# Kernel optimization log

Hardware: AMD Instinct MI355X
Metric: run time of the kernel (lower is better)

Reference implementation:

```python
import jax, jax.numpy as jnp
import numpy as np

B, T, D_IN, D_OUT = 4, 2048, 1024, 1024

def setup_inputs() -> dict:
    key = jax.random.key(0)
    k1, k2, k3, k4 = jax.random.split(key, 4)
    return {
        "vector": jax.random.normal(k1, (B, T, D_IN), dtype=jnp.float32),
        "W_queries": jax.random.normal(k2, (D_IN, D_OUT), dtype=jnp.float32),
        "W_keys": jax.random.normal(k3, (D_IN, D_OUT), dtype=jnp.float32),
        "W_values": jax.random.normal(k4, (D_IN, D_OUT), dtype=jnp.float32),
    }

def reference(vector, W_queries, W_keys, W_values):
    # vector: [B,T,d_in]; projections -> [B,T,d_out]
    q = vector @ W_queries
    k = vector @ W_keys
    v = vector @ W_values
    d_out = k.shape[-1]
    scores = jnp.einsum('btd,bsd->bts', q, k)  # [B,T,T]
    t = scores.shape[1]
    causal = jnp.tril(jnp.ones((t, t), dtype=bool))  # True = keep (mask is triu diag=1)
    scores = jnp.where(causal, scores, -jnp.inf)
    weights = jax.nn.softmax(scores / jnp.sqrt(jnp.float32(d_out)), axis=-1)
    # dropout p=0.0 -> identity
    return jnp.einsum('bts,bsd->btd', weights, v)
```

## Files before the change

### kernel.cpp

```cpp
#include <hip/hip_runtime.h>

#define TT   2048
#define DD   1024
#define BK   32

typedef float  f32x4  __attribute__((ext_vector_type(4)));
typedef __bf16 bf16x8 __attribute__((ext_vector_type(8)));

static __device__ __forceinline__ unsigned short f2bf(float f){
  unsigned int u = __float_as_uint(f);
  return (unsigned short)((u + 0x7fffu + ((u >> 16) & 1u)) >> 16);
}
static __device__ __forceinline__ float bf2f(unsigned short h){
  return __uint_as_float(((unsigned int)h) << 16);
}
static __device__ __forceinline__ bf16x8 ld8(const unsigned short* p){
  return *(const bf16x8*)p;
}
static __device__ __forceinline__ f32x4 mfma16(bf16x8 a, bf16x8 b, f32x4 c){
  return __builtin_amdgcn_mfma_f32_16x16x32_bf16(a, b, c, 0, 0, 0);
}

static __device__ __forceinline__ void async16(
    const unsigned short* g, unsigned short* l)
{
  __builtin_amdgcn_global_load_lds(
      (const __attribute__((address_space(1))) unsigned int*)g,
      (__attribute__((address_space(3))) unsigned int*)l, 16, 0, 0);
}

static __device__ __forceinline__ void stage_async(
    const unsigned short* __restrict__ src, int row_stride,
    unsigned short* __restrict__ dst, int t)
{
#pragma unroll
  for (int j = 0; j < 2; j++){
    int e = (t + j * 256) * 8;
    int row = e >> 5, col = e & 31;
    async16(src + (size_t)row * row_stride + col, dst + e);
  }
}

__global__ __launch_bounds__(256) void split_all_kernel(
    const float* __restrict__ X,  const float* __restrict__ Wq,
    const float* __restrict__ Wk, const float* __restrict__ Wv,
    unsigned short* __restrict__ Xhi,  unsigned short* __restrict__ Xlo,
    unsigned short* __restrict__ Wqhi, unsigned short* __restrict__ Wqlo,
    unsigned short* __restrict__ Wkhi, unsigned short* __restrict__ Wklo,
    unsigned short* __restrict__ WvThi)
{
  __shared__ float tile[32][33];
  int bx = blockIdx.x;
  if (bx < 10240){
    const float* src; unsigned short *hi, *lo; size_t base;
    if (bx < 8192)      { src = X;  hi = Xhi;  lo = Xlo;  base = (size_t)bx * 1024; }
    else if (bx < 9216) { src = Wq; hi = Wqhi; lo = Wqlo; base = (size_t)(bx - 8192) * 1024; }
    else                { src = Wk; hi = Wkhi; lo = Wklo; base = (size_t)(bx - 9216) * 1024; }
    size_t i = base + (size_t)threadIdx.x * 4;
    const float4 x = *(const float4*)(src + i);
    ushort4 h, l;
    h.x = f2bf(x.x); l.x = f2bf(x.x - bf2f(h.x));
    h.y = f2bf(x.y); l.y = f2bf(x.y - bf2f(h.y));
    h.z = f2bf(x.z); l.z = f2bf(x.z - bf2f(h.z));
    h.w = f2bf(x.w); l.w = f2bf(x.w - bf2f(h.w));
    *(ushort4*)(hi + i) = h;
    *(ushort4*)(lo + i) = l;
  } else {
    int tid = bx - 10240;
    int k0 = (tid & 31) * 32, n0 = (tid >> 5) * 32;
    int tx = threadIdx.x & 31, ty = threadIdx.x >> 5;
#pragma unroll
    for (int r = 0; r < 4; r++){
      int row = ty + r * 8;
      tile[row][tx] = Wv[(size_t)(k0 + row) * DD + n0 + tx];
    }
    __syncthreads();
#pragma unroll
    for (int r = 0; r < 4; r++){
      int nrow = ty + r * 8;
      float v = tile[tx][nrow];
      WvThi[(size_t)(n0 + nrow) * DD + k0 + tx] = f2bf(v);
    }
  }
}

__global__ __launch_bounds__(256) void mt_kernel(
    const unsigned short* __restrict__ Wkhi, const unsigned short* __restrict__ Wklo,
    const unsigned short* __restrict__ Wqhi, const unsigned short* __restrict__ Wqlo,
    unsigned short* __restrict__ MThi, unsigned short* __restrict__ MTlo)
{
  __shared__ unsigned short Ahi[128 * BK], Alo[128 * BK];
  __shared__ unsigned short Bhi[128 * BK], Blo[128 * BK];
  int e0 = blockIdx.y * 128, d0 = blockIdx.x * 128;
  const unsigned short* Ah_g = Wkhi + (size_t)e0 * DD;
  const unsigned short* Al_g = Wklo + (size_t)e0 * DD;
  const unsigned short* Bh_g = Wqhi + (size_t)d0 * DD;
  const unsigned short* Bl_g = Wqlo + (size_t)d0 * DD;
  int t = threadIdx.x;
  int lane = t & 63, w = t >> 6;
  int mw = (w >> 1) << 6, nw = (w & 1) << 6;
  int frow = lane & 15, fk = (lane >> 4) << 3;

  f32x4 acc[4][4];
#pragma unroll
  for (int a = 0; a < 4; a++)
#pragma unroll
    for (int c = 0; c < 4; c++){ f32x4 zz = {0.f,0.f,0.f,0.f}; acc[a][c] = zz; }

  for (int kk = 0; kk < DD / BK; kk++){
    int k0 = kk * BK;
    stage_async(Ah_g + k0, DD, Ahi, t);
    stage_async(Al_g + k0, DD, Alo, t);
    stage_async(Bh_g + k0, DD, Bhi, t);
    stage_async(Bl_g + k0, DD, Blo, t);
    __syncthreads();

    bf16x8 ah[4], al[4], bh[4], bl[4];
#pragma unroll
    for (int tm = 0; tm < 4; tm++){
      int off = (mw + tm * 16 + frow) * BK + fk;
      ah[tm] = ld8(&Ahi[off]); al[tm] = ld8(&Alo[off]);
    }
#pragma unroll
    for (int tn = 0; tn < 4; tn++){
      int off = (nw + tn * 16 + frow) * BK + fk;
      bh[tn] = ld8(&Bhi[off]); bl[tn] = ld8(&Blo[off]);
    }
#pragma unroll
    for (int tm = 0; tm < 4; tm++)
#pragma unroll
      for (int tn = 0; tn < 4; tn++){
        acc[tm][tn] = mfma16(ah[tm], bh[tn], acc[tm][tn]);
        acc[tm][tn] = mfma16(ah[tm], bl[tn], acc[tm][tn]);
        acc[tm][tn] = mfma16(al[tm], bh[tn], acc[tm][tn]);
      }
    __syncthreads();
  }

#pragma unroll
  for (int tm = 0; tm < 4; tm++)
#pragma unroll
    for (int tn = 0; tn < 4; tn++)
#pragma unroll
      for (int r = 0; r < 4; r++){
        float v = acc[tm][tn][r];
        int ge = e0 + mw + tm * 16 + ((lane >> 4) << 2) + r;
        int gd = d0 + nw + tn * 16 + frow;
        size_t idx = (size_t)ge * DD + gd;
        unsigned short h = f2bf(v);
        MThi[idx] = h; MTlo[idx] = f2bf(v - bf2f(h));
      }
}

__global__ __launch_bounds__(256, 2) void y_kernel(
    const unsigned short* __restrict__ Xhi, const unsigned short* __restrict__ Xlo,
    const unsigned short* __restrict__ MThi, const unsigned short* __restrict__ MTlo,
    const unsigned short* __restrict__ WvThi,
    unsigned short* __restrict__ Yhi, unsigned short* __restrict__ Ylo,
    unsigned short* __restrict__ VT)
{
  __shared__ unsigned short Ahs[128 * BK], Als[128 * BK];
  __shared__ unsigned short Bmh[128 * BK], Bml[128 * BK], Bvh[128 * BK];
  int m0 = blockIdx.x * 128, n0 = blockIdx.y * 128;
  const unsigned short* Ah_g  = Xhi   + (size_t)m0 * DD;
  const unsigned short* Al_g  = Xlo   + (size_t)m0 * DD;
  const unsigned short* Bmh_g = MThi  + (size_t)n0 * DD;
  const unsigned short* Bml_g = MTlo  + (size_t)n0 * DD;
  const unsigned short* Bvh_g = WvThi + (size_t)n0 * DD;
  int t = threadIdx.x;
  int lane = t & 63, w = t >> 6;
  int mw = (w >> 1) << 6, nw = (w & 1) << 6;
  int frow = lane & 15, fk = (lane >> 4) << 3;

  f32x4 accY[4][4], accV[4][4];
#pragma unroll
  for (int a = 0; a < 4; a++)
#pragma unroll
    for (int c = 0; c < 4; c++){
      f32x4 zz = {0.f,0.f,0.f,0.f}; accY[a][c] = zz; accV[a][c] = zz;
    }

  for (int kk = 0; kk < DD / BK; kk++){
    int k0 = kk * BK;
    stage_async(Ah_g  + k0, DD, Ahs, t);
    stage_async(Al_g  + k0, DD, Als, t);
    stage_async(Bmh_g + k0, DD, Bmh, t);
    stage_async(Bml_g + k0, DD, Bml, t);
    stage_async(Bvh_g + k0, DD, Bvh, t);
    __syncthreads();

    bf16x8 ah[4], al[4];
#pragma unroll
    for (int tm = 0; tm < 4; tm++){
      int off = (mw + tm * 16 + frow) * BK + fk;
      ah[tm] = ld8(&Ahs[off]); al[tm] = ld8(&Als[off]);
    }
#pragma unroll
    for (int tn = 0; tn < 4; tn++){
      int off = (nw + tn * 16 + frow) * BK + fk;
      bf16x8 bmh = ld8(&Bmh[off]), bml = ld8(&Bml[off]), bvh = ld8(&Bvh[off]);
#pragma unroll
      for (int tm = 0; tm < 4; tm++){
        accY[tm][tn] = mfma16(ah[tm], bmh, accY[tm][tn]);
        accY[tm][tn] = mfma16(ah[tm], bml, accY[tm][tn]);
        accY[tm][tn] = mfma16(al[tm], bmh, accY[tm][tn]);
        accV[tm][tn] = mfma16(ah[tm], bvh, accV[tm][tn]);
      }
    }
    __syncthreads();
  }

#pragma unroll
  for (int tm = 0; tm < 4; tm++)
#pragma unroll
    for (int tn = 0; tn < 4; tn++)
#pragma unroll
      for (int r = 0; r < 4; r++){
        int grow = m0 + mw + tm * 16 + ((lane >> 4) << 2) + r;
        int gcol = n0 + nw + tn * 16 + frow;
        size_t idx = (size_t)grow * DD + gcol;
        float vy = accY[tm][tn][r];
        unsigned short hy = f2bf(vy);
        Yhi[idx] = hy; Ylo[idx] = f2bf(vy - bf2f(hy));
        int b = grow >> 11, tl = grow & 2047;
        VT[((size_t)(b * DD + gcol) << 11) | tl] = f2bf(accV[tm][tn][r]);
      }
}

__global__ __launch_bounds__(256) void s_kernel(
    const unsigned short* __restrict__ Yhi, const unsigned short* __restrict__ Ylo,
    const unsigned short* __restrict__ Xhi, const unsigned short* __restrict__ Xlo,
    float* __restrict__ S, float* __restrict__ Spart)
{
  __shared__ unsigned short Ahi[128 * BK], Alo[128 * BK];
  __shared__ unsigned short Bhi[128 * BK], Blo[128 * BK];
  int bx = blockIdx.x;
  int u, q, kbeg, kend;
  if (bx < 512){ u = bx; q = 0; kbeg = 0; kend = 32; }
  else {
    int e = bx - 512;
    q = e & 3;
    u = 512 + (e >> 2);
    kbeg = q * 8; kend = kbeg + 8;
  }
  int b = u & 3;
  int tid = u >> 2;
  int bi = (int)((sqrtf(8.f * (float)tid + 1.f) - 1.f) * 0.5f);
  while ((bi + 1) * (bi + 2) / 2 <= tid) bi++;
  while (bi * (bi + 1) / 2 > tid) bi--;
  int bj = tid - bi * (bi + 1) / 2;
  int i0 = bi * 128, j0 = bj * 128;
  const unsigned short* Ah_g = Yhi + (size_t)(b * TT + i0) * DD;
  const unsigned short* Al_g = Ylo + (size_t)(b * TT + i0) * DD;
  const unsigned short* Bh_g = Xhi + (size_t)(b * TT + j0) * DD;
  const unsigned short* Bl_g = Xlo + (size_t)(b * TT + j0) * DD;
  int t = threadIdx.x;
  int lane = t & 63, w = t >> 6;
  int mw = (w >> 1) << 6, nw = (w & 1) << 6;
  int frow = lane & 15, fk = (lane >> 4) << 3;

  f32x4 acc[4][4];
#pragma unroll
  for (int a = 0; a < 4; a++)
#pragma unroll
    for (int c = 0; c < 4; c++){ f32x4 zz = {0.f,0.f,0.f,0.f}; acc[a][c] = zz; }

  for (int kk = kbeg; kk < kend; kk++){
    int k0 = kk * BK;
    stage_async(Ah_g + k0, DD, Ahi, t);
    stage_async(Al_g + k0, DD, Alo, t);
    stage_async(Bh_g + k0, DD, Bhi, t);
    stage_async(Bl_g + k0, DD, Blo, t);
    __syncthreads();

    bf16x8 ah[4], al[4], bh[4], bl[4];
#pragma unroll
    for (int tm = 0; tm < 4; tm++){
      int off = (mw + tm * 16 + frow) * BK + fk;
      ah[tm] = ld8(&Ahi[off]); al[tm] = ld8(&Alo[off]);
    }
#pragma unroll
    for (int tn = 0; tn < 4; tn++){
      int off = (nw + tn * 16 + frow) * BK + fk;
      bh[tn] = ld8(&Bhi[off]); bl[tn] = ld8(&Blo[off]);
    }
#pragma unroll
    for (int tm = 0; tm < 4; tm++)
#pragma unroll
      for (int tn = 0; tn < 4; tn++){
        acc[tm][tn] = mfma16(ah[tm], bh[tn], acc[tm][tn]);
        acc[tm][tn] = mfma16(ah[tm], bl[tn], acc[tm][tn]);
        acc[tm][tn] = mfma16(al[tm], bh[tn], acc[tm][tn]);
      }
    __syncthreads();
  }

  if (q == 0){
#pragma unroll
    for (int tm = 0; tm < 4; tm++)
#pragma unroll
      for (int tn = 0; tn < 4; tn++)
#pragma unroll
        for (int r = 0; r < 4; r++){
          int gi = i0 + mw + tm * 16 + ((lane >> 4) << 2) + r;
          int gj = j0 + nw + tn * 16 + frow;
          S[((size_t)(b * TT + gi) * TT) + gj] = acc[tm][tn][r] * 0.03125f;
        }
  } else {
    float* dst = Spart + ((size_t)(q - 1) * 32 + (u - 512)) * 16384;
#pragma unroll
    for (int tm = 0; tm < 4; tm++)
#pragma unroll
      for (int tn = 0; tn < 4; tn++)
#pragma unroll
        for (int r = 0; r < 4; r++){
          int row = mw + tm * 16 + ((lane >> 4) << 2) + r;
          int col = nw + tn * 16 + frow;
          dst[row * 128 + col] = acc[tm][tn][r] * 0.03125f;
        }
  }
}

__global__ __launch_bounds__(256) void softmax_kernel(
    const float* __restrict__ S, const float* __restrict__ Spart,
    unsigned short* __restrict__ P)
{
  int i = blockIdx.x, b = blockIdx.y;
  const float* s = S + (size_t)(b * TT + i) * TT;
  unsigned short* p = P + (size_t)(b * TT + i) * TT;
  int n = i + 1;
  int npad = ((i >> 7) + 1) << 7;
  int t = threadIdx.x;
  bool qrow = (i >= 1920);
  __shared__ float red[256];

  float v[8];
  float mx = -1e30f;
#pragma unroll
  for (int pas = 0; pas < 2; pas++){
    int idx = t * 4 + pas * 1024;
    float4 x = *(const float4*)(s + idx);
    if (qrow && pas == 1){
      int jt = (idx - 1024) >> 7;
      int qt = 4 * jt + b;
      size_t base = (size_t)qt * 16384 + (size_t)(i - 1920) * 128 + ((idx - 1024) & 127);
      const float4 p1 = *(const float4*)(Spart + base);
      const float4 p2 = *(const float4*)(Spart + 32 * 16384 + base);
      const float4 p3 = *(const float4*)(Spart + 2 * 32 * 16384 + base);
      x.x += p1.x + p2.x + p3.x;
      x.y += p1.y + p2.y + p3.y;
      x.z += p1.z + p2.z + p3.z;
      x.w += p1.w + p2.w + p3.w;
    }
    v[pas*4+0] = (idx + 0 < n) ? x.x : -1e30f;
    v[pas*4+1] = (idx + 1 < n) ? x.y : -1e30f;
    v[pas*4+2] = (idx + 2 < n) ? x.z : -1e30f;
    v[pas*4+3] = (idx + 3 < n) ? x.w : -1e30f;
#pragma unroll
    for (int e = 0; e < 4; e++) mx = fmaxf(mx, v[pas*4+e]);
  }
  red[t] = mx; __syncthreads();
  for (int k = 128; k > 0; k >>= 1){ if (t < k) red[t] = fmaxf(red[t], red[t + k]); __syncthreads(); }
  mx = red[0]; __syncthreads();

  float sum = 0.f;
#pragma unroll
  for (int j = 0; j < 8; j++){
    v[j] = __expf(v[j] - mx);
    sum += v[j];
  }
  red[t] = sum; __syncthreads();
  for (int k = 128; k > 0; k >>= 1){ if (t < k) red[t] += red[t + k]; __syncthreads(); }
  float inv = 1.0f / red[0];

#pragma unroll
  for (int pas = 0; pas < 2; pas++){
    int idx = t * 4 + pas * 1024;
    if (idx < npad){
      ushort4 o;
      o.x = f2bf(v[pas*4+0] * inv);
      o.y = f2bf(v[pas*4+1] * inv);
      o.z = f2bf(v[pas*4+2] * inv);
      o.w = f2bf(v[pas*4+3] * inv);
      *(ushort4*)(p + idx) = o;
    }
  }
}

__global__ __launch_bounds__(256) void pv_kernel(
    const unsigned short* __restrict__ P, const unsigned short* __restrict__ VT,
    float* __restrict__ O)
{
  __shared__ unsigned short At[128 * BK];
  __shared__ unsigned short Bt[128 * BK];
  int b  = blockIdx.z;
  int by = (int)gridDim.y - 1 - blockIdx.y;
  int i0 = by * 128, n0 = blockIdx.x * 128;
  int ksteps = (by + 1) * 4;
  const unsigned short* A_g = P  + (size_t)(b * TT + i0) * TT;
  const unsigned short* B_g = VT + (size_t)(b * DD + n0) * TT;
  int t = threadIdx.x;
  int lane = t & 63, w = t >> 6;
  int mw = (w >> 1) << 6, nw = (w & 1) << 6;
  int frow = lane & 15, fk = (lane >> 4) << 3;

  f32x4 acc[4][4];
#pragma unroll
  for (int a = 0; a < 4; a++)
#pragma unroll
    for (int c = 0; c < 4; c++){ f32x4 zz = {0.f,0.f,0.f,0.f}; acc[a][c] = zz; }

  for (int kk = 0; kk < ksteps; kk++){
    int k0 = kk * BK;
    stage_async(A_g + k0, TT, At, t);
    stage_async(B_g + k0, TT, Bt, t);
    __syncthreads();

    bf16x8 af[4], bf[4];
#pragma unroll
    for (int tm = 0; tm < 4; tm++) af[tm] = ld8(&At[(mw + tm * 16 + frow) * BK + fk]);
#pragma unroll
    for (int tn = 0; tn < 4; tn++) bf[tn] = ld8(&Bt[(nw + tn * 16 + frow) * BK + fk]);
#pragma unroll
    for (int tm = 0; tm < 4; tm++)
#pragma unroll
      for (int tn = 0; tn < 4; tn++)
        acc[tm][tn] = mfma16(af[tm], bf[tn], acc[tm][tn]);
    __syncthreads();
  }

#pragma unroll
  for (int tm = 0; tm < 4; tm++)
#pragma unroll
    for (int tn = 0; tn < 4; tn++)
#pragma unroll
      for (int r = 0; r < 4; r++){
        int gi = i0 + mw + tm * 16 + ((lane >> 4) << 2) + r;
        int gd = n0 + nw + tn * 16 + frow;
        O[(size_t)(b * TT + gi) * DD + gd] = acc[tm][tn][r];
      }
}

extern "C" void kernel_launch(void* const* d_in, const int* in_sizes, int n_in,
                              void* d_out, int out_size, void* d_ws, size_t ws_size,
                              hipStream_t stream) {
  const float* X  = (const float*)d_in[0];
  const float* Wq = (const float*)d_in[1];
  const float* Wk = (const float*)d_in[2];
  const float* Wv = (const float*)d_in[3];
  float* Out = (float*)d_out;

  const size_t M1 = 1048576u;
  unsigned short* base  = (unsigned short*)d_ws;
  unsigned short* Wqhi  = base;
  unsigned short* Wqlo  = base + 1 * M1;
  unsigned short* Wkhi  = base + 2 * M1;
  unsigned short* Wklo  = base + 3 * M1;
  unsigned short* WvThi = base + 4 * M1;
  unsigned short* MThi  = base + 5 * M1;
  unsigned short* MTlo  = base + 6 * M1;
  unsigned short* Xhi   = base + 7 * M1;
  unsigned short* Xlo   = base + 15 * M1;
  unsigned short* Yhi   = base + 23 * M1;
  unsigned short* Ylo   = base + 31 * M1;
  unsigned short* VT    = base + 39 * M1;
  float*          S     = (float*)(base + 47 * M1);
  float*          Spart = (float*)(base + 79 * M1);
  unsigned short* P     = Xhi;

  dim3 blk(256);
  split_all_kernel<<<dim3(11264), blk, 0, stream>>>(X, Wq, Wk, Wv,
      Xhi, Xlo, Wqhi, Wqlo, Wkhi, Wklo, WvThi);
  mt_kernel<<<dim3(8, 8), blk, 0, stream>>>(Wkhi, Wklo, Wqhi, Wqlo, MThi, MTlo);
  y_kernel<<<dim3(64, 8), blk, 0, stream>>>(Xhi, Xlo, MThi, MTlo, WvThi, Yhi, Ylo, VT);
  s_kernel<<<dim3(640), blk, 0, stream>>>(Yhi, Ylo, Xhi, Xlo, S, Spart);
  softmax_kernel<<<dim3(2048, 4, 1), blk, 0, stream>>>(S, Spart, P);
  pv_kernel<<<dim3(8, 16, 4), blk, 0, stream>>>(P, VT, Out);
}
```

Baseline: 340.8 us.

## Stage V-transpose through LDS for coalesced stores; process two K-steps per pv iteration

In y_kernel the shared buffers become one pool. The V projection tile is written transposed into it with padded stride 132, then copied out as contiguous ushort4 rows of VT, replacing scattered 2-byte strided global stores. In pv_kernel each iteration stages two BK slices into separate buffers, halving the number of barriers per K range at the cost of doubled LDS use. ksteps is always a multiple of 4, so the pairing needs no remainder handling.

```diff
diff --git a/kernel.cpp b/kernel.cpp
--- a/kernel.cpp
+++ b/kernel.cpp
@@ -159,8 +159,12 @@
     unsigned short* __restrict__ Yhi, unsigned short* __restrict__ Ylo,
     unsigned short* __restrict__ VT)
 {
-  __shared__ unsigned short Ahs[128 * BK], Als[128 * BK];
-  __shared__ unsigned short Bmh[128 * BK], Bml[128 * BK], Bvh[128 * BK];
+  __shared__ unsigned short pool[20480];
+  unsigned short* Ahs = pool;
+  unsigned short* Als = pool + 4096;
+  unsigned short* Bmh = pool + 8192;
+  unsigned short* Bml = pool + 12288;
+  unsigned short* Bvh = pool + 16384;
   int m0 = blockIdx.x * 128, n0 = blockIdx.y * 128;
   const unsigned short* Ah_g  = Xhi   + (size_t)m0 * DD;
   const unsigned short* Al_g  = Xlo   + (size_t)m0 * DD;
@@ -222,9 +226,32 @@
         float vy = accY[tm][tn][r];
         unsigned short hy = f2bf(vy);
         Yhi[idx] = hy; Ylo[idx] = f2bf(vy - bf2f(hy));
-        int b = grow >> 11, tl = grow & 2047;
-        VT[((size_t)(b * DD + gcol) << 11) | tl] = f2bf(accV[tm][tn][r]);
       }
+
+#pragma unroll
+  for (int tm = 0; tm < 4; tm++)
+#pragma unroll
+    for (int tn = 0; tn < 4; tn++){
+      int row = mw + tm * 16 + ((lane >> 4) << 2);
+      int col = nw + tn * 16 + frow;
+      ushort4 v4;
+      v4.x = f2bf(accV[tm][tn][0]);
+      v4.y = f2bf(accV[tm][tn][1]);
+      v4.z = f2bf(accV[tm][tn][2]);
+      v4.w = f2bf(accV[tm][tn][3]);
+      *(ushort4*)&pool[col * 132 + row] = v4;
+    }
+  __syncthreads();
+  {
+    int colx = t >> 1;
+    int r0 = (t & 1) << 6;
+    int b = m0 >> 11;
+    size_t vbase = (((size_t)(b * DD + n0 + colx)) << 11) | ((size_t)(m0 & 2047) + r0);
+    const unsigned short* srcl = &pool[colx * 132 + r0];
+#pragma unroll
+    for (int r = 0; r < 64; r += 4)
+      *(ushort4*)&VT[vbase + r] = *(const ushort4*)&srcl[r];
+  }
 }
 
 __global__ __launch_bounds__(256) void s_kernel(
@@ -391,8 +418,8 @@
     const unsigned short* __restrict__ P, const unsigned short* __restrict__ VT,
     float* __restrict__ O)
 {
-  __shared__ unsigned short At[128 * BK];
-  __shared__ unsigned short Bt[128 * BK];
+  __shared__ unsigned short At0[128 * BK], At1[128 * BK];
+  __shared__ unsigned short Bt0[128 * BK], Bt1[128 * BK];
   int b  = blockIdx.z;
   int by = (int)gridDim.y - 1 - blockIdx.y;
   int i0 = by * 128, n0 = blockIdx.x * 128;
@@ -410,17 +437,28 @@
 #pragma unroll
     for (int c = 0; c < 4; c++){ f32x4 zz = {0.f,0.f,0.f,0.f}; acc[a][c] = zz; }
 
-  for (int kk = 0; kk < ksteps; kk++){
+  for (int kk = 0; kk < ksteps; kk += 2){
     int k0 = kk * BK;
-    stage_async(A_g + k0, TT, At, t);
-    stage_async(B_g + k0, TT, Bt, t);
+    stage_async(A_g + k0, TT, At0, t);
+    stage_async(A_g + k0 + BK, TT, At1, t);
+    stage_async(B_g + k0, TT, Bt0, t);
+    stage_async(B_g + k0 + BK, TT, Bt1, t);
     __syncthreads();
 
     bf16x8 af[4], bf[4];
 #pragma unroll
-    for (int tm = 0; tm < 4; tm++) af[tm] = ld8(&At[(mw + tm * 16 + frow) * BK + fk]);
-#pragma unroll
-    for (int tn = 0; tn < 4; tn++) bf[tn] = ld8(&Bt[(nw + tn * 16 + frow) * BK + fk]);
+    for (int tm = 0; tm < 4; tm++) af[tm] = ld8(&At0[(mw + tm * 16 + frow) * BK + fk]);
+#pragma unroll
+    for (int tn = 0; tn < 4; tn++) bf[tn] = ld8(&Bt0[(nw + tn * 16 + frow) * BK + fk]);
+#pragma unroll
+    for (int tm = 0; tm < 4; tm++)
+#pragma unroll
+      for (int tn = 0; tn < 4; tn++)
+        acc[tm][tn] = mfma16(af[tm], bf[tn], acc[tm][tn]);
+#pragma unroll
+    for (int tm = 0; tm < 4; tm++) af[tm] = ld8(&At1[(mw + tm * 16 + frow) * BK + fk]);
+#pragma unroll
+    for (int tn = 0; tn < 4; tn++) bf[tn] = ld8(&Bt1[(nw + tn * 16 + frow) * BK + fk]);
 #pragma unroll
     for (int tm = 0; tm < 4; tm++)
 #pragma unroll
```

Result: faster. 327.4 us (-3.9%).
